# Optimization experiments

Hardware: AMD Instinct MI355X
Metric: run time of the kernel (lower is better)

The kernel has to match this reference:

```python
import jax, jax.numpy as jnp
import numpy as np

N_GAUSS = 2048
HEIGHT = 192
WIDTH = 192
ALPHA_MAX = 0.999
ALPHA_MIN = 1.0 / 255.0


def setup_inputs() -> dict:
    key = jax.random.key(0)
    k1, k2, k3, k4, k5, k6 = jax.random.split(key, 6)
    # 2D means in pixel coords
    means2d = jax.random.uniform(k1, (N_GAUSS, 2)) * jnp.array([WIDTH, HEIGHT], jnp.float32)
    depths = jax.random.uniform(k2, (N_GAUSS,)) * 10.0 + 0.1
    # build positive-definite 2x2 pixel-space covariances -> conics (inverse cov)
    scales = jax.random.uniform(k3, (N_GAUSS, 2)) * 6.0 + 1.0  # std 1..7 px
    theta = jax.random.uniform(k4, (N_GAUSS,)) * (2.0 * np.pi)
    c, s = jnp.cos(theta), jnp.sin(theta)
    s0, s1 = scales[:, 0] ** 2, scales[:, 1] ** 2
    cxx = c * c * s0 + s * s * s1
    cyy = s * s * s0 + c * c * s1
    cxy = c * s * (s0 - s1)
    det = cxx * cyy - cxy * cxy
    conics = jnp.stack([cyy / det, -cxy / det, cxx / det], axis=-1)  # [a,b,c]
    colors = jax.random.uniform(k5, (N_GAUSS, 3))
    opacities = jax.random.uniform(k6, (N_GAUSS,)) * 0.9 + 0.05
    background = jnp.zeros((3,), jnp.float32)
    return {"means2d": means2d, "conics": conics, "colors": colors,
            "opacities": opacities, "depths": depths, "background": background}


def reference(means2d, conics, colors, opacities, depths, background):
    # depth sort (front to back), as gsplat's tile sort does globally per image
    order = jnp.argsort(depths)
    means2d = means2d[order]
    conics = conics[order]
    colors = colors[order]
    opacities = opacities[order]

    # pixel centers, flattened to P = H*W
    ys, xs = jnp.meshgrid(jnp.arange(HEIGHT, dtype=jnp.float32) + 0.5,
                          jnp.arange(WIDTH, dtype=jnp.float32) + 0.5,
                          indexing="ij")
    px = xs.reshape(-1)  # [P]
    py = ys.reshape(-1)

    dx = px[None, :] - means2d[:, 0:1]  # [N, P]
    dy = py[None, :] - means2d[:, 1:2]
    a, b, cc = conics[:, 0:1], conics[:, 1:2], conics[:, 2:3]
    # gsplat 2DGS fallback: sigma = 0.5*(A dx^2 + C dy^2) + B dx dy
    sigma = 0.5 * (a * dx * dx + cc * dy * dy) + b * dx * dy
    alpha = jnp.minimum(ALPHA_MAX, opacities[:, None] * jnp.exp(-sigma))
    alpha = jnp.where((sigma > 0.0) & (alpha >= ALPHA_MIN), alpha, 0.0)

    one_minus = 1.0 - alpha
    trans = jnp.cumprod(one_minus, axis=0)  # inclusive
    # exclusive transmittance before each gaussian
    T = jnp.concatenate([jnp.ones((1, alpha.shape[1]), alpha.dtype), trans[:-1]], axis=0)
    w = T * alpha  # [N, P] compositing weights
    rgb = jnp.einsum("np,nc->cp", w, colors)  # [3, P]
    T_final = trans[-1]  # [P]
    img = rgb + background[:, None] * T_final[None, :]
    return img.reshape(3, HEIGHT, WIDTH)
```

## Files before the change

kernel.cpp:

```cpp
#include <hip/hip_runtime.h>
#include <hip/hip_bf16.h>

#define NG 2048
#define IMW 192
#define IMH 192
#define NSEG 8
#define SEGSZ (NG / NSEG)

__device__ float4 g_cull[NG];
__device__ float4 g_dat[NG * 2];

__device__ __forceinline__ float bf2f(unsigned short u) {
    union { unsigned int i; float f; } v;
    v.i = ((unsigned int)u) << 16;
    return v.f;
}

__device__ __forceinline__ unsigned short f2bf(float f) {
    union { float f; unsigned int i; } v;
    v.f = f;
    unsigned int x = v.i;
    unsigned int r = (x + 0x7fffu + ((x >> 16) & 1u)) >> 16;
    return (unsigned short)r;
}

__device__ __forceinline__ bool probe_is_f32_wave(const unsigned short* dus, int lane) {
    float v = bf2f(dus[lane & 63]);
    bool bad = !(v >= 0.05f && v <= 16.0f);
    return __ballot(bad) != 0ull;
}

__global__ __launch_bounds__(256) void sort_gather_kernel(
    const void* __restrict__ means2d_,
    const void* __restrict__ conics_,
    const void* __restrict__ colors_,
    const void* __restrict__ opac_,
    const void* __restrict__ depths_)
{
    __shared__ int s_part[4][64];
    const int t  = threadIdx.x;
    const int il = t & 63;
    const int q  = t >> 6;
    const int i  = blockIdx.x * 64 + il;

    const unsigned short* dus = (const unsigned short*)depths_;
    const bool is_f32 = probe_is_f32_wave(dus, t);

    int rank = 0;
    if (is_f32) {
        const float* df = (const float*)depths_;
        const float di = df[i];
        const int base = q * 512;
#pragma unroll 8
        for (int m = 0; m < 512; ++m) {
            float dj = df[base + m];
            rank += (dj < di || (dj == di && (base + m) < i)) ? 1 : 0;
        }
    } else {
        const unsigned int my_key = (((unsigned int)dus[i]) << 16) | (unsigned int)i;
        const unsigned int* d2 = (const unsigned int*)depths_;
        const int base = q * 256;
#pragma unroll 8
        for (int m = 0; m < 256; ++m) {
            unsigned int w = d2[base + m];
            unsigned int j = (unsigned int)((base + m) << 1);
            unsigned int k0 = (w << 16) | j;
            unsigned int k1 = (w & 0xffff0000u) | (j + 1u);
            rank += (k0 < my_key) ? 1 : 0;
            rank += (k1 < my_key) ? 1 : 0;
        }
    }
    s_part[q][il] = rank;
    __syncthreads();

    if (t < 64) {
        const int g = blockIdx.x * 64 + t;
        const int r = s_part[0][t] + s_part[1][t] + s_part[2][t] + s_part[3][t];

        float mx, my, ca, cb, cc, r0, g0, b0, op;
        if (is_f32) {
            const float* mf = (const float*)means2d_;
            const float* cf = (const float*)conics_;
            const float* lf = (const float*)colors_;
            const float* of = (const float*)opac_;
            mx = mf[2 * g + 0]; my = mf[2 * g + 1];
            ca = cf[3 * g + 0]; cb = cf[3 * g + 1]; cc = cf[3 * g + 2];
            r0 = lf[3 * g + 0]; g0 = lf[3 * g + 1]; b0 = lf[3 * g + 2];
            op = of[g];
        } else {
            const unsigned short* mu = (const unsigned short*)means2d_;
            const unsigned short* cu = (const unsigned short*)conics_;
            const unsigned short* lu = (const unsigned short*)colors_;
            const unsigned short* ou = (const unsigned short*)opac_;
            mx = bf2f(mu[2 * g + 0]); my = bf2f(mu[2 * g + 1]);
            ca = bf2f(cu[3 * g + 0]); cb = bf2f(cu[3 * g + 1]); cc = bf2f(cu[3 * g + 2]);
            r0 = bf2f(lu[3 * g + 0]); g0 = bf2f(lu[3 * g + 1]); b0 = bf2f(lu[3 * g + 2]);
            op = bf2f(ou[g]);
        }

        const float det = ca * cc - cb * cb;
        const float tau = __logf(255.0f * op);
        float rxp, ryp;
        if (det > 1e-12f && tau > 0.0f) {
            float s = 2.0f * tau / det;
            rxp = __fsqrt_rn(fmaxf(s * cc, 0.0f)) + 3.5f + 0.05f;
            ryp = __fsqrt_rn(fmaxf(s * ca, 0.0f)) + 3.5f + 0.05f;
        } else if (tau <= 0.0f) {
            rxp = -1e9f; ryp = -1e9f;
        } else {
            rxp = 1e9f;  ryp = 1e9f;
        }

        const float L2E = 1.44269504088896f;
        g_cull[r] = make_float4(mx, my, rxp, ryp);
        g_dat[2 * r + 0] = make_float4(0.5f * ca * L2E, cb * L2E, 0.5f * cc * L2E, __log2f(op));
        g_dat[2 * r + 1] = make_float4(r0, g0, b0, 0.0f);
    }
}

__global__ __launch_bounds__(512) void render_kernel(
    const void* __restrict__ depths_,
    const void* __restrict__ background_,
    void* __restrict__ out_)
{
    __shared__ float4 scomb[NSEG][64];
    const int t    = threadIdx.x;
    const int lane = t & 63;
    const int wave = t >> 6;
    const bool is_f32 = probe_is_f32_wave((const unsigned short*)depths_, lane);

    const int bx = blockIdx.x % 24;
    const int by = blockIdx.x / 24;
    const int x = bx * 8 + (lane & 7);
    const int y = by * 8 + (lane >> 3);
    const float px = (float)x + 0.5f;
    const float py = (float)y + 0.5f;
    const float cx = (float)(bx * 8) + 4.0f;
    const float cy = (float)(by * 8) + 4.0f;

    float T = 1.0f, accr = 0.0f, accg = 0.0f, accb = 0.0f;

    const int segBase = wave * SEGSZ;
#pragma unroll
    for (int b = 0; b < SEGSZ / 64; ++b) {
        const int base = segBase + b * 64;
        const float4 cu = g_cull[base + lane];
        const bool hit = (__builtin_fabsf(cu.x - cx) <= cu.z) &&
                         (__builtin_fabsf(cu.y - cy) <= cu.w);
        unsigned long long mask = __ballot(hit);
        while (mask) {
            const int j = __builtin_ctzll(mask);
            mask &= mask - 1;
            const float mx = __shfl(cu.x, j, 64);
            const float my = __shfl(cu.y, j, 64);
            const float4 d0 = g_dat[2 * (base + j) + 0];
            const float4 d1 = g_dat[2 * (base + j) + 1];
            const float dx = px - mx;
            const float dy = py - my;
            const float sp = fmaf(d0.x * dx, dx, fmaf(d0.z * dy, dy, d0.y * dx * dy));
            const float e = d0.w - sp;
            const float alpha = __builtin_amdgcn_exp2f(e);
            const bool ok = (sp > 0.0f) && (e >= -7.9943534f);
            const float w = ok ? T * alpha : 0.0f;
            accr = fmaf(w, d1.x, accr);
            accg = fmaf(w, d1.y, accg);
            accb = fmaf(w, d1.z, accb);
            T -= w;
        }
        if (__ballot(T > 1e-4f) == 0ull) break;
    }

    scomb[wave][lane] = make_float4(accr, accg, accb, T);
    __syncthreads();

    if (wave == 0) {
        float4 c0 = scomb[0][lane];
        float Cr = c0.x, Cg = c0.y, Cb = c0.z, Tr = c0.w;
#pragma unroll
        for (int w = 1; w < NSEG; ++w) {
            float4 cw = scomb[w][lane];
            Cr = fmaf(Tr, cw.x, Cr);
            Cg = fmaf(Tr, cw.y, Cg);
            Cb = fmaf(Tr, cw.z, Cb);
            Tr *= cw.w;
        }

        const int pix = y * IMW + x;
        if (is_f32) {
            const float* bg = (const float*)background_;
            float* out = (float*)out_;
            out[0 * IMH * IMW + pix] = fmaf(bg[0], Tr, Cr);
            out[1 * IMH * IMW + pix] = fmaf(bg[1], Tr, Cg);
            out[2 * IMH * IMW + pix] = fmaf(bg[2], Tr, Cb);
        } else {
            const unsigned short* bg = (const unsigned short*)background_;
            unsigned short* out = (unsigned short*)out_;
            out[0 * IMH * IMW + pix] = f2bf(fmaf(bf2f(bg[0]), Tr, Cr));
            out[1 * IMH * IMW + pix] = f2bf(fmaf(bf2f(bg[1]), Tr, Cg));
            out[2 * IMH * IMW + pix] = f2bf(fmaf(bf2f(bg[2]), Tr, Cb));
        }
    }
}

extern "C" void kernel_launch(void* const* d_in, const int* in_sizes, int n_in,
                              void* d_out, int out_size, void* d_ws, size_t ws_size,
                              hipStream_t stream)
{
    sort_gather_kernel<<<32, 256, 0, stream>>>(d_in[0], d_in[1], d_in[2], d_in[3], d_in[4]);
    render_kernel<<<576, 512, 0, stream>>>(d_in[4], d_in[5], d_out);
}
```

Baseline: 87.02 us.

## Stage hit gaussians in LDS, prefetch cull data, widen rank-sort blocks

The render kernel now compacts each 64-gaussian batch's hits into a per-wave LDS buffer. Hit lanes load their gaussian data in parallel instead of the serial per-hit global loads and shuffles. It also prefetches the next batch's cull record and loosens the early-termination threshold from 1e-4 to 1e-3. The sort kernel doubles its threads per block so each rank-counting thread scans half as many depths. The threshold change alters numerics slightly, and the larger LDS footprint may reduce occupancy.

```diff
diff --git a/kernel.cpp b/kernel.cpp
--- a/kernel.cpp
+++ b/kernel.cpp
@@ -6,6 +6,7 @@
 #define IMH 192
 #define NSEG 8
 #define SEGSZ (NG / NSEG)
+#define NB (SEGSZ / 64)
 
 __device__ float4 g_cull[NG];
 __device__ float4 g_dat[NG * 2];
@@ -30,14 +31,14 @@
     return __ballot(bad) != 0ull;
 }
 
-__global__ __launch_bounds__(256) void sort_gather_kernel(
+__global__ __launch_bounds__(512) void sort_gather_kernel(
     const void* __restrict__ means2d_,
     const void* __restrict__ conics_,
     const void* __restrict__ colors_,
     const void* __restrict__ opac_,
     const void* __restrict__ depths_)
 {
-    __shared__ int s_part[4][64];
+    __shared__ int s_part[8][64];
     const int t  = threadIdx.x;
     const int il = t & 63;
     const int q  = t >> 6;
@@ -50,18 +51,18 @@
     if (is_f32) {
         const float* df = (const float*)depths_;
         const float di = df[i];
-        const int base = q * 512;
+        const int base = q * 256;
 #pragma unroll 8
-        for (int m = 0; m < 512; ++m) {
+        for (int m = 0; m < 256; ++m) {
             float dj = df[base + m];
             rank += (dj < di || (dj == di && (base + m) < i)) ? 1 : 0;
         }
     } else {
         const unsigned int my_key = (((unsigned int)dus[i]) << 16) | (unsigned int)i;
         const unsigned int* d2 = (const unsigned int*)depths_;
-        const int base = q * 256;
+        const int base = q * 128;
 #pragma unroll 8
-        for (int m = 0; m < 256; ++m) {
+        for (int m = 0; m < 128; ++m) {
             unsigned int w = d2[base + m];
             unsigned int j = (unsigned int)((base + m) << 1);
             unsigned int k0 = (w << 16) | j;
@@ -75,7 +76,9 @@
 
     if (t < 64) {
         const int g = blockIdx.x * 64 + t;
-        const int r = s_part[0][t] + s_part[1][t] + s_part[2][t] + s_part[3][t];
+        int r = 0;
+#pragma unroll
+        for (int k = 0; k < 8; ++k) r += s_part[k][t];
 
         float mx, my, ca, cb, cc, r0, g0, b0, op;
         if (is_f32) {
@@ -123,6 +126,7 @@
     const void* __restrict__ background_,
     void* __restrict__ out_)
 {
+    __shared__ float4 s_hit[NSEG][64 * 3];
     __shared__ float4 scomb[NSEG][64];
     const int t    = threadIdx.x;
     const int lane = t & 63;
@@ -138,36 +142,52 @@
     const float cx = (float)(bx * 8) + 4.0f;
     const float cy = (float)(by * 8) + 4.0f;
 
+    float4* hitbuf = s_hit[wave];
     float T = 1.0f, accr = 0.0f, accg = 0.0f, accb = 0.0f;
 
     const int segBase = wave * SEGSZ;
+    float4 cu = g_cull[segBase + lane];
 #pragma unroll
-    for (int b = 0; b < SEGSZ / 64; ++b) {
+    for (int b = 0; b < NB; ++b) {
         const int base = segBase + b * 64;
-        const float4 cu = g_cull[base + lane];
+        float4 cu_next = cu;
+        if (b + 1 < NB) cu_next = g_cull[base + 64 + lane];
+
         const bool hit = (__builtin_fabsf(cu.x - cx) <= cu.z) &&
                          (__builtin_fabsf(cu.y - cy) <= cu.w);
-        unsigned long long mask = __ballot(hit);
-        while (mask) {
-            const int j = __builtin_ctzll(mask);
-            mask &= mask - 1;
-            const float mx = __shfl(cu.x, j, 64);
-            const float my = __shfl(cu.y, j, 64);
-            const float4 d0 = g_dat[2 * (base + j) + 0];
-            const float4 d1 = g_dat[2 * (base + j) + 1];
-            const float dx = px - mx;
-            const float dy = py - my;
-            const float sp = fmaf(d0.x * dx, dx, fmaf(d0.z * dy, dy, d0.y * dx * dy));
-            const float e = d0.w - sp;
-            const float alpha = __builtin_amdgcn_exp2f(e);
-            const bool ok = (sp > 0.0f) && (e >= -7.9943534f);
-            const float w = ok ? T * alpha : 0.0f;
-            accr = fmaf(w, d1.x, accr);
-            accg = fmaf(w, d1.y, accg);
-            accb = fmaf(w, d1.z, accb);
-            T -= w;
-        }
-        if (__ballot(T > 1e-4f) == 0ull) break;
+        const unsigned long long mask = __ballot(hit);
+        const int nh = __popcll(mask);
+        if (nh) {
+            if (hit) {
+                const int slot = __popcll(mask & ((1ull << lane) - 1ull));
+                const float4 d0 = g_dat[2 * (base + lane) + 0];
+                const float4 d1 = g_dat[2 * (base + lane) + 1];
+                hitbuf[slot * 3 + 0] = cu;
+                hitbuf[slot * 3 + 1] = d0;
+                hitbuf[slot * 3 + 2] = d1;
+            }
+            __asm__ volatile("s_waitcnt lgkmcnt(0)" ::: "memory");
+            __builtin_amdgcn_wave_barrier();
+
+            for (int k = 0; k < nh; ++k) {
+                const float4 h0 = hitbuf[k * 3 + 0];
+                const float4 h1 = hitbuf[k * 3 + 1];
+                const float4 h2 = hitbuf[k * 3 + 2];
+                const float dx = px - h0.x;
+                const float dy = py - h0.y;
+                const float sp = fmaf(h1.x * dx, dx, fmaf(h1.z * dy, dy, h1.y * dx * dy));
+                const float e = h1.w - sp;
+                const float alpha = __builtin_amdgcn_exp2f(e);
+                const bool ok = (sp > 0.0f) && (e >= -7.9943534f);
+                const float w = ok ? T * alpha : 0.0f;
+                accr = fmaf(w, h2.x, accr);
+                accg = fmaf(w, h2.y, accg);
+                accb = fmaf(w, h2.z, accb);
+                T -= w;
+            }
+            if (__ballot(T > 1e-3f) == 0ull) break;
+        }
+        cu = cu_next;
     }
 
     scomb[wave][lane] = make_float4(accr, accg, accb, T);
@@ -206,6 +226,6 @@
                               void* d_out, int out_size, void* d_ws, size_t ws_size,
                               hipStream_t stream)
 {
-    sort_gather_kernel<<<32, 256, 0, stream>>>(d_in[0], d_in[1], d_in[2], d_in[3], d_in[4]);
+    sort_gather_kernel<<<32, 512, 0, stream>>>(d_in[0], d_in[1], d_in[2], d_in[3], d_in[4]);
     render_kernel<<<576, 512, 0, stream>>>(d_in[4], d_in[5], d_out);
 }
```

Result: faster. 79.45 us (-8.7%).

## Fuse sort and render into one kernel with per-tile culling and local rank sort

Applied to the files above, without the earlier changes.

Removes the global sort/gather kernel. Each 8x8 tile block now culls all gaussians against its own tile, appends the survivors' depth|index keys to shared memory with an atomic counter, and rank-sorts only that culled list. It then stages sorted payloads in chunks of 256 into LDS and composites them across 8 waves, with a running blend and an early stop. This saves a launch and the global intermediate buffers, but every block repeats the culling of all 2048 gaussians, runs an O(n^2) rank sort over its list, and pays more block-wide barriers.

```diff
diff --git a/kernel.cpp b/kernel.cpp
--- a/kernel.cpp
+++ b/kernel.cpp
@@ -4,11 +4,7 @@
 #define NG 2048
 #define IMW 192
 #define IMH 192
-#define NSEG 8
-#define SEGSZ (NG / NSEG)
-
-__device__ float4 g_cull[NG];
-__device__ float4 g_dat[NG * 2];
+#define CHUNK 256
 
 __device__ __forceinline__ float bf2f(unsigned short u) {
     union { unsigned int i; float f; } v;
@@ -30,174 +26,188 @@
     return __ballot(bad) != 0ull;
 }
 
-__global__ __launch_bounds__(256) void sort_gather_kernel(
+__global__ __launch_bounds__(512) void fused_render_kernel(
     const void* __restrict__ means2d_,
     const void* __restrict__ conics_,
     const void* __restrict__ colors_,
     const void* __restrict__ opac_,
-    const void* __restrict__ depths_)
-{
-    __shared__ int s_part[4][64];
-    const int t  = threadIdx.x;
-    const int il = t & 63;
-    const int q  = t >> 6;
-    const int i  = blockIdx.x * 64 + il;
-
-    const unsigned short* dus = (const unsigned short*)depths_;
-    const bool is_f32 = probe_is_f32_wave(dus, t);
-
-    int rank = 0;
-    if (is_f32) {
-        const float* df = (const float*)depths_;
-        const float di = df[i];
-        const int base = q * 512;
-#pragma unroll 8
-        for (int m = 0; m < 512; ++m) {
-            float dj = df[base + m];
-            rank += (dj < di || (dj == di && (base + m) < i)) ? 1 : 0;
-        }
-    } else {
-        const unsigned int my_key = (((unsigned int)dus[i]) << 16) | (unsigned int)i;
-        const unsigned int* d2 = (const unsigned int*)depths_;
-        const int base = q * 256;
-#pragma unroll 8
-        for (int m = 0; m < 256; ++m) {
-            unsigned int w = d2[base + m];
-            unsigned int j = (unsigned int)((base + m) << 1);
-            unsigned int k0 = (w << 16) | j;
-            unsigned int k1 = (w & 0xffff0000u) | (j + 1u);
-            rank += (k0 < my_key) ? 1 : 0;
-            rank += (k1 < my_key) ? 1 : 0;
-        }
-    }
-    s_part[q][il] = rank;
-    __syncthreads();
-
-    if (t < 64) {
-        const int g = blockIdx.x * 64 + t;
-        const int r = s_part[0][t] + s_part[1][t] + s_part[2][t] + s_part[3][t];
-
-        float mx, my, ca, cb, cc, r0, g0, b0, op;
-        if (is_f32) {
-            const float* mf = (const float*)means2d_;
-            const float* cf = (const float*)conics_;
-            const float* lf = (const float*)colors_;
-            const float* of = (const float*)opac_;
-            mx = mf[2 * g + 0]; my = mf[2 * g + 1];
-            ca = cf[3 * g + 0]; cb = cf[3 * g + 1]; cc = cf[3 * g + 2];
-            r0 = lf[3 * g + 0]; g0 = lf[3 * g + 1]; b0 = lf[3 * g + 2];
-            op = of[g];
-        } else {
-            const unsigned short* mu = (const unsigned short*)means2d_;
-            const unsigned short* cu = (const unsigned short*)conics_;
-            const unsigned short* lu = (const unsigned short*)colors_;
-            const unsigned short* ou = (const unsigned short*)opac_;
-            mx = bf2f(mu[2 * g + 0]); my = bf2f(mu[2 * g + 1]);
-            ca = bf2f(cu[3 * g + 0]); cb = bf2f(cu[3 * g + 1]); cc = bf2f(cu[3 * g + 2]);
-            r0 = bf2f(lu[3 * g + 0]); g0 = bf2f(lu[3 * g + 1]); b0 = bf2f(lu[3 * g + 2]);
-            op = bf2f(ou[g]);
-        }
-
-        const float det = ca * cc - cb * cb;
-        const float tau = __logf(255.0f * op);
-        float rxp, ryp;
-        if (det > 1e-12f && tau > 0.0f) {
-            float s = 2.0f * tau / det;
-            rxp = __fsqrt_rn(fmaxf(s * cc, 0.0f)) + 3.5f + 0.05f;
-            ryp = __fsqrt_rn(fmaxf(s * ca, 0.0f)) + 3.5f + 0.05f;
-        } else if (tau <= 0.0f) {
-            rxp = -1e9f; ryp = -1e9f;
-        } else {
-            rxp = 1e9f;  ryp = 1e9f;
-        }
-
-        const float L2E = 1.44269504088896f;
-        g_cull[r] = make_float4(mx, my, rxp, ryp);
-        g_dat[2 * r + 0] = make_float4(0.5f * ca * L2E, cb * L2E, 0.5f * cc * L2E, __log2f(op));
-        g_dat[2 * r + 1] = make_float4(r0, g0, b0, 0.0f);
-    }
-}
-
-__global__ __launch_bounds__(512) void render_kernel(
     const void* __restrict__ depths_,
     const void* __restrict__ background_,
     void* __restrict__ out_)
 {
-    __shared__ float4 scomb[NSEG][64];
+    __shared__ unsigned long long s_keys[NG];
+    __shared__ float4 s_pay[CHUNK * 3];
+    __shared__ float4 s_comb[8][64];
+    __shared__ float4 s_run[64];
+    __shared__ unsigned int s_cnt;
+    __shared__ int s_stop;
+
     const int t    = threadIdx.x;
     const int lane = t & 63;
     const int wave = t >> 6;
-    const bool is_f32 = probe_is_f32_wave((const unsigned short*)depths_, lane);
+    const unsigned short* dus = (const unsigned short*)depths_;
+    const bool is_f32 = probe_is_f32_wave(dus, lane);
 
     const int bx = blockIdx.x % 24;
     const int by = blockIdx.x / 24;
+    const float cx = (float)(bx * 8) + 4.0f;
+    const float cy = (float)(by * 8) + 4.0f;
     const int x = bx * 8 + (lane & 7);
     const int y = by * 8 + (lane >> 3);
     const float px = (float)x + 0.5f;
     const float py = (float)y + 0.5f;
-    const float cx = (float)(bx * 8) + 4.0f;
-    const float cy = (float)(by * 8) + 4.0f;
-
-    float T = 1.0f, accr = 0.0f, accg = 0.0f, accb = 0.0f;
-
-    const int segBase = wave * SEGSZ;
+
+    if (t == 0) { s_cnt = 0u; s_stop = 0; }
+    if (t < 64) s_run[t] = make_float4(0.f, 0.f, 0.f, 1.f);
+    __syncthreads();
+
 #pragma unroll
-    for (int b = 0; b < SEGSZ / 64; ++b) {
-        const int base = segBase + b * 64;
-        const float4 cu = g_cull[base + lane];
-        const bool hit = (__builtin_fabsf(cu.x - cx) <= cu.z) &&
-                         (__builtin_fabsf(cu.y - cy) <= cu.w);
-        unsigned long long mask = __ballot(hit);
-        while (mask) {
-            const int j = __builtin_ctzll(mask);
-            mask &= mask - 1;
-            const float mx = __shfl(cu.x, j, 64);
-            const float my = __shfl(cu.y, j, 64);
-            const float4 d0 = g_dat[2 * (base + j) + 0];
-            const float4 d1 = g_dat[2 * (base + j) + 1];
-            const float dx = px - mx;
-            const float dy = py - my;
-            const float sp = fmaf(d0.x * dx, dx, fmaf(d0.z * dy, dy, d0.y * dx * dy));
-            const float e = d0.w - sp;
+    for (int k = 0; k < NG / 512; ++k) {
+        const int g = t + k * 512;
+        float mx, my, ca, cb, cc, op;
+        unsigned int dbits;
+        if (is_f32) {
+            const float* mf = (const float*)means2d_;
+            const float* cf = (const float*)conics_;
+            const float* of = (const float*)opac_;
+            const unsigned int* du = (const unsigned int*)depths_;
+            mx = mf[2 * g]; my = mf[2 * g + 1];
+            ca = cf[3 * g]; cb = cf[3 * g + 1]; cc = cf[3 * g + 2];
+            op = of[g];
+            dbits = du[g];
+        } else {
+            const unsigned short* mu = (const unsigned short*)means2d_;
+            const unsigned short* cu = (const unsigned short*)conics_;
+            const unsigned short* ou = (const unsigned short*)opac_;
+            mx = bf2f(mu[2 * g]); my = bf2f(mu[2 * g + 1]);
+            ca = bf2f(cu[3 * g]); cb = bf2f(cu[3 * g + 1]); cc = bf2f(cu[3 * g + 2]);
+            op = bf2f(ou[g]);
+            dbits = ((unsigned int)dus[g]) << 16;
+        }
+
+        const float det = ca * cc - cb * cb;
+        const float tau = __logf(255.0f * op);
+        bool hit;
+        if (det > 1e-12f && tau > 0.0f) {
+            const float s = 2.0f * tau / det;
+            const float rx = __fsqrt_rn(fmaxf(s * cc, 0.0f)) + 3.55f;
+            const float ry = __fsqrt_rn(fmaxf(s * ca, 0.0f)) + 3.55f;
+            hit = (__builtin_fabsf(mx - cx) <= rx) && (__builtin_fabsf(my - cy) <= ry);
+        } else if (tau <= 0.0f) {
+            hit = false;
+        } else {
+            hit = true;
+        }
+        if (hit) {
+            const unsigned int slot = atomicAdd(&s_cnt, 1u);
+            s_keys[slot] = (((unsigned long long)dbits) << 32) | (unsigned long long)g;
+        }
+    }
+    __syncthreads();
+    const int n = (int)s_cnt;
+
+    unsigned long long mykey[NG / 512];
+    int myrank[NG / 512];
+    int nit = 0;
+    for (int i = t; i < n; i += 512) { mykey[nit] = s_keys[i]; myrank[nit] = 0; ++nit; }
+    if (nit) {
+        for (int k = 0; k < n; ++k) {
+            const unsigned long long kk = s_keys[k];
+#pragma unroll
+            for (int j = 0; j < NG / 512; ++j)
+                if (j < nit) myrank[j] += (kk < mykey[j]) ? 1 : 0;
+        }
+    }
+    __syncthreads();
+    for (int j = 0; j < nit; ++j) s_keys[myrank[j]] = mykey[j];
+    __syncthreads();
+
+    const float L2E = 1.44269504088896f;
+    for (int cb0 = 0; cb0 < n; cb0 += CHUNK) {
+        const int m = min(CHUNK, n - cb0);
+
+        if (t < m) {
+            const int g = (int)(s_keys[cb0 + t] & 0xffffffffull);
+            float mx, my, ca, cb, cc, op, r0, g0, b0;
+            if (is_f32) {
+                const float* mf = (const float*)means2d_;
+                const float* cf = (const float*)conics_;
+                const float* lf = (const float*)colors_;
+                const float* of = (const float*)opac_;
+                mx = mf[2 * g]; my = mf[2 * g + 1];
+                ca = cf[3 * g]; cb = cf[3 * g + 1]; cc = cf[3 * g + 2];
+                r0 = lf[3 * g]; g0 = lf[3 * g + 1]; b0 = lf[3 * g + 2];
+                op = of[g];
+            } else {
+                const unsigned short* mu = (const unsigned short*)means2d_;
+                const unsigned short* cu = (const unsigned short*)conics_;
+                const unsigned short* lu = (const unsigned short*)colors_;
+                const unsigned short* ou = (const unsigned short*)opac_;
+                mx = bf2f(mu[2 * g]); my = bf2f(mu[2 * g + 1]);
+                ca = bf2f(cu[3 * g]); cb = bf2f(cu[3 * g + 1]); cc = bf2f(cu[3 * g + 2]);
+                r0 = bf2f(lu[3 * g]); g0 = bf2f(lu[3 * g + 1]); b0 = bf2f(lu[3 * g + 2]);
+                op = bf2f(ou[g]);
+            }
+            s_pay[t * 3 + 0] = make_float4(mx, my, 0.f, 0.f);
+            s_pay[t * 3 + 1] = make_float4(0.5f * ca * L2E, cb * L2E, 0.5f * cc * L2E, __log2f(op));
+            s_pay[t * 3 + 2] = make_float4(r0, g0, b0, 0.f);
+        }
+        __syncthreads();
+
+        const int lo = wave * (CHUNK / 8);
+        const int hi = min(lo + CHUNK / 8, m);
+        float T = 1.0f, ar = 0.f, ag = 0.f, ab = 0.f;
+        for (int k = lo; k < hi; ++k) {
+            const float4 h0 = s_pay[k * 3 + 0];
+            const float4 h1 = s_pay[k * 3 + 1];
+            const float4 h2 = s_pay[k * 3 + 2];
+            const float dx = px - h0.x;
+            const float dy = py - h0.y;
+            const float sp = fmaf(h1.x * dx, dx, fmaf(h1.z * dy, dy, h1.y * dx * dy));
+            const float e = h1.w - sp;
             const float alpha = __builtin_amdgcn_exp2f(e);
             const bool ok = (sp > 0.0f) && (e >= -7.9943534f);
             const float w = ok ? T * alpha : 0.0f;
-            accr = fmaf(w, d1.x, accr);
-            accg = fmaf(w, d1.y, accg);
-            accb = fmaf(w, d1.z, accb);
+            ar = fmaf(w, h2.x, ar);
+            ag = fmaf(w, h2.y, ag);
+            ab = fmaf(w, h2.z, ab);
             T -= w;
         }
-        if (__ballot(T > 1e-4f) == 0ull) break;
-    }
-
-    scomb[wave][lane] = make_float4(accr, accg, accb, T);
-    __syncthreads();
-
-    if (wave == 0) {
-        float4 c0 = scomb[0][lane];
-        float Cr = c0.x, Cg = c0.y, Cb = c0.z, Tr = c0.w;
+        s_comb[wave][lane] = make_float4(ar, ag, ab, T);
+        __syncthreads();
+
+        if (t < 64) {
+            float4 R = s_run[t];
 #pragma unroll
-        for (int w = 1; w < NSEG; ++w) {
-            float4 cw = scomb[w][lane];
-            Cr = fmaf(Tr, cw.x, Cr);
-            Cg = fmaf(Tr, cw.y, Cg);
-            Cb = fmaf(Tr, cw.z, Cb);
-            Tr *= cw.w;
-        }
-
+            for (int w = 0; w < 8; ++w) {
+                const float4 c = s_comb[w][t];
+                R.x = fmaf(R.w, c.x, R.x);
+                R.y = fmaf(R.w, c.y, R.y);
+                R.z = fmaf(R.w, c.z, R.z);
+                R.w *= c.w;
+            }
+            s_run[t] = R;
+            if (__ballot(R.w > 1e-3f) == 0ull && t == 0) s_stop = 1;
+        }
+        __syncthreads();
+        if (s_stop) break;
+    }
+
+    if (t < 64) {
+        const float4 R = s_run[t];
         const int pix = y * IMW + x;
         if (is_f32) {
             const float* bg = (const float*)background_;
             float* out = (float*)out_;
-            out[0 * IMH * IMW + pix] = fmaf(bg[0], Tr, Cr);
-            out[1 * IMH * IMW + pix] = fmaf(bg[1], Tr, Cg);
-            out[2 * IMH * IMW + pix] = fmaf(bg[2], Tr, Cb);
+            out[0 * IMH * IMW + pix] = fmaf(bg[0], R.w, R.x);
+            out[1 * IMH * IMW + pix] = fmaf(bg[1], R.w, R.y);
+            out[2 * IMH * IMW + pix] = fmaf(bg[2], R.w, R.z);
         } else {
             const unsigned short* bg = (const unsigned short*)background_;
             unsigned short* out = (unsigned short*)out_;
-            out[0 * IMH * IMW + pix] = f2bf(fmaf(bf2f(bg[0]), Tr, Cr));
-            out[1 * IMH * IMW + pix] = f2bf(fmaf(bf2f(bg[1]), Tr, Cg));
-            out[2 * IMH * IMW + pix] = f2bf(fmaf(bf2f(bg[2]), Tr, Cb));
+            out[0 * IMH * IMW + pix] = f2bf(fmaf(bf2f(bg[0]), R.w, R.x));
+            out[1 * IMH * IMW + pix] = f2bf(fmaf(bf2f(bg[1]), R.w, R.y));
+            out[2 * IMH * IMW + pix] = f2bf(fmaf(bf2f(bg[2]), R.w, R.z));
         }
     }
 }
@@ -206,6 +216,6 @@
                               void* d_out, int out_size, void* d_ws, size_t ws_size,
                               hipStream_t stream)
 {
-    sort_gather_kernel<<<32, 256, 0, stream>>>(d_in[0], d_in[1], d_in[2], d_in[3], d_in[4]);
-    render_kernel<<<576, 512, 0, stream>>>(d_in[4], d_in[5], d_out);
-}
+    fused_render_kernel<<<576, 512, 0, stream>>>(
+        d_in[0], d_in[1], d_in[2], d_in[3], d_in[4], d_in[5], d_out);
+}
```

Result: faster. 74.50 us (-14.4%).
